# Kernel optimization log

Hardware: AMD Instinct MI355X
Metric: run time of the kernel (lower is better)

Reference implementation:

```python
import jax, jax.numpy as jnp
import numpy as np

NUM_EMBEDDINGS = 1024
EMBEDDING_DIM = 128
COMMITMENT_COST = 0.25


def setup_inputs() -> dict:
    key = jax.random.key(0)
    k_in, k_cb = jax.random.split(key)
    inputs = jax.random.normal(k_in, (8, EMBEDDING_DIM, 16, 32, 32), dtype=jnp.float32)
    # torch init: uniform_(-1/num_embeddings, 1/num_embeddings)
    codebook = jax.random.uniform(
        k_cb, (NUM_EMBEDDINGS, EMBEDDING_DIM), dtype=jnp.float32,
        minval=-1.0 / NUM_EMBEDDINGS, maxval=1.0 / NUM_EMBEDDINGS)
    return {"inputs": inputs, "codebook": codebook}


def reference(inputs, codebook):
    # inputs: [B, C, D, H, W] with C == embedding_dim; codebook: [K, C]
    C = codebook.shape[1]
    flat = jnp.transpose(inputs, (0, 2, 3, 4, 1)).reshape(-1, C)  # [N, C]
    # squared L2 distances via the expanded form (matches torch code)
    distances = (jnp.sum(flat ** 2, axis=1, keepdims=True)
                 + jnp.sum(codebook ** 2, axis=1)
                 - 2.0 * flat @ codebook.T)  # [N, K]
    encoding_indices = jnp.argmin(distances, axis=1)  # [N]
    quantized = codebook[encoding_indices]  # [N, C]
    # NOTE: faithful to original bug — plain reshape back to channels-first
    # inputs.shape with no inverse permute (torch: quantized.view(inputs.shape))
    quantized = quantized.reshape(inputs.shape)
    e_latent_loss = jnp.mean((jax.lax.stop_gradient(quantized) - inputs) ** 2)
    q_latent_loss = jnp.mean((quantized - jax.lax.stop_gradient(inputs)) ** 2)
    loss = q_latent_loss + COMMITMENT_COST * e_latent_loss
    # straight-through estimator
    quantized_st = inputs + jax.lax.stop_gradient(quantized - inputs)
    return quantized_st, loss, encoding_indices
```

## Files before the change

kernel.cpp:

```cpp
#include <hip/hip_runtime.h>

typedef unsigned short u16;
typedef __attribute__((ext_vector_type(8))) short bf16x8;
typedef __attribute__((ext_vector_type(4))) float f32x4;

#define K_CB  1024
#define N_ROWS 131072
#define NUMEL (N_ROWS * 128)
#define TAU2 6.0e-4f
#define SMALLCAP 32768
#define FULLCAP  32768

#define GLOAD16(gp, lp) __builtin_amdgcn_global_load_lds( \
    (const __attribute__((address_space(1))) unsigned int*)(gp), \
    (__attribute__((address_space(3))) unsigned int*)(lp), 16, 0, 0)

__device__ __forceinline__ u16 f2bf(float x) {
    union { float f; unsigned int u; } a; a.f = x;
    unsigned int r = a.u + 0x7fffu + ((a.u >> 16) & 1u);
    return (u16)(r >> 16);
}

__global__ void prep_cb_kernel(const float* __restrict__ cb, float* __restrict__ bn,
                               u16* __restrict__ Bpl, int* __restrict__ cnts) {
    int k = blockIdx.x * 256 + threadIdx.x;
    if (blockIdx.x == 0 && threadIdx.x < 2) cnts[threadIdx.x] = 0;
    if (k >= K_CB) return;
    const float4* row4 = reinterpret_cast<const float4*>(cb) + k * 32;
    float s = 0.f;
    #pragma unroll
    for (int i = 0; i < 32; ++i) {
        float4 v = row4[i];
        s = fmaf(v.x, v.x, s); s = fmaf(v.y, v.y, s);
        s = fmaf(v.z, v.z, s); s = fmaf(v.w, v.w, s);
    }
    bn[k] = s;
    const float* rf = cb + k * 128;
    #pragma unroll
    for (int s8 = 0; s8 < 16; ++s8) {
        unsigned int hw[8];
        #pragma unroll
        for (int j = 0; j < 8; ++j) hw[j] = f2bf(rf[s8 * 8 + j]);
        uint4 H;
        H.x = hw[0] | (hw[1] << 16); H.y = hw[2] | (hw[3] << 16);
        H.z = hw[4] | (hw[5] << 16); H.w = hw[6] | (hw[7] << 16);
        *reinterpret_cast<uint4*>(&Bpl[((size_t)s8 * 1024 + k) * 8]) = H;
    }
}

__launch_bounds__(256, 3)
__global__ void gemm_fused_kernel(const float* __restrict__ in, const float* __restrict__ cb,
                                  const u16* __restrict__ Bpl, const float* __restrict__ bn,
                                  float* __restrict__ out_q, float* __restrict__ idx_out,
                                  uint2* __restrict__ smallL, int* __restrict__ fullL,
                                  int* __restrict__ cnts,
                                  float* __restrict__ deltas, float* __restrict__ partials) {
    __shared__ u16 A_s[16 * 64 * 8];
    __shared__ u16 Bb[2 * 4 * 256 * 8];
    __shared__ float bn_s[K_CB];
    __shared__ float red_s[4];

    const int tid = threadIdx.x;
    const int w = tid >> 6, lane = tid & 63, g4 = lane >> 4, l15 = lane & 15;
    const int blk = blockIdx.x, n0 = blk * 64;

    #pragma unroll
    for (int i = 0; i < 4; ++i) {
        const u16* g = Bpl + (size_t)(w * 1024 + i * 64 + lane) * 8;
        GLOAD16(g, &Bb[(w * 256 + i * 64) * 8]);
    }
    for (int i = tid; i < K_CB; i += 256) bn_s[i] = bn[i];

    {
        const int base = (n0 >> 14) * (128 * 16384) + (n0 & 16383);
        #pragma unroll
        for (int i = 0; i < 4; ++i) {
            int p = tid + i * 256;
            int n = p & 63, s = p >> 6;
            const float* g = in + base + (size_t)(s * 8) * 16384 + n;
            unsigned int pw[8];
            #pragma unroll
            for (int j = 0; j < 8; ++j) pw[j] = f2bf(g[(size_t)j * 16384]);
            uint4 H;
            H.x = pw[0] | (pw[1] << 16); H.y = pw[2] | (pw[3] << 16);
            H.z = pw[4] | (pw[5] << 16); H.w = pw[6] | (pw[7] << 16);
            *reinterpret_cast<uint4*>(&A_s[(s * 64 + n) * 8]) = H;
        }
    }
    __syncthreads();

    f32x4 acc[4][4];
    const f32x4 zz = {0.f, 0.f, 0.f, 0.f};
    #pragma unroll
    for (int mi = 0; mi < 4; ++mi)
        #pragma unroll
        for (int ni = 0; ni < 4; ++ni) acc[mi][ni] = zz;

    float b1[16], b2[16]; int i1[16];
    #pragma unroll
    for (int sl = 0; sl < 16; ++sl) { b1[sl] = 3.4e38f; b2[sl] = 3.4e38f; i1[sl] = 0; }

    #pragma unroll
    for (int t = 0; t < 16; ++t) {
        const int chunk = t >> 2, cc = t & 3, buf = t & 1;
        if (t < 15) {
            const int t2 = t + 1, chunk2 = t2 >> 2, cc2 = t2 & 3, nb = t2 & 1;
            #pragma unroll
            for (int i = 0; i < 4; ++i) {
                const u16* g = Bpl + (size_t)((cc2 * 4 + w) * 1024 + chunk2 * 256 + i * 64 + lane) * 8;
                GLOAD16(g, &Bb[((nb * 4 + w) * 256 + i * 64) * 8]);
            }
        }
        bf16x8 af[4], bfr[4];
        #pragma unroll
        for (int mi = 0; mi < 4; ++mi)
            af[mi] = *reinterpret_cast<const bf16x8*>(
                &A_s[((cc * 4 + g4) * 64 + mi * 16 + l15) * 8]);
        #pragma unroll
        for (int ni = 0; ni < 4; ++ni)
            bfr[ni] = *reinterpret_cast<const bf16x8*>(
                &Bb[((buf * 4 + g4) * 256 + w * 64 + ni * 16 + l15) * 8]);
        #pragma unroll
        for (int mi = 0; mi < 4; ++mi)
            #pragma unroll
            for (int ni = 0; ni < 4; ++ni)
                acc[mi][ni] = __builtin_amdgcn_mfma_f32_16x16x32_bf16(af[mi], bfr[ni], acc[mi][ni], 0, 0, 0);

        if (cc == 3) {
            const int cb0s = chunk * 256;
            #pragma unroll
            for (int mi = 0; mi < 4; ++mi) {
                #pragma unroll
                for (int ni = 0; ni < 4; ++ni) {
                    int n = cb0s + w * 64 + ni * 16 + l15;
                    float bnv = bn_s[n];
                    #pragma unroll
                    for (int r = 0; r < 4; ++r) {
                        float s = fmaf(-2.0f, acc[mi][ni][r], bnv);
                        int sl = mi * 4 + r;
                        if (s < b1[sl]) { b2[sl] = b1[sl]; b1[sl] = s; i1[sl] = n; }
                        else if (s < b2[sl]) b2[sl] = s;
                    }
                    acc[mi][ni] = zz;
                }
            }
        }
        __syncthreads();
    }

    float* m_b1   = (float*)Bb;
    float* m_b2   = m_b1 + 256;
    int*   m_i1   = (int*)(m_b2 + 256);
    int*   idx_s  = m_i1 + 256;
    float* gmin_s = (float*)(idx_s + 64);
    int*   flg_s  = (int*)(gmin_s + 64);
    int*   ccnt_s = flg_s + 64;
    int*   fb_s   = ccnt_s + 64;
    int*   cand_s = fb_s + 64;

    #pragma unroll
    for (int sl = 0; sl < 16; ++sl) {
        float v1 = b1[sl], v2 = b2[sl]; int ix = i1[sl];
        #pragma unroll
        for (int m = 1; m < 16; m <<= 1) {
            float o1 = __shfl_xor(v1, m, 64);
            int   oi = __shfl_xor(ix, m, 64);
            float o2 = __shfl_xor(v2, m, 64);
            if (o1 < v1 || (o1 == v1 && oi < ix)) { v2 = fminf(v1, o2); v1 = o1; ix = oi; }
            else v2 = fminf(v2, o1);
        }
        if (l15 == 0) {
            int mi = sl >> 2, r = sl & 3;
            int rl = mi * 16 + g4 * 4 + r;
            m_b1[w * 64 + rl] = v1; m_b2[w * 64 + rl] = v2; m_i1[w * 64 + rl] = ix;
        }
    }
    __syncthreads();
    if (tid < 64) {
        float v1 = m_b1[tid], v2 = m_b2[tid]; int ix = m_i1[tid];
        #pragma unroll
        for (int wv = 1; wv < 4; ++wv) {
            float o1 = m_b1[wv * 64 + tid], o2 = m_b2[wv * 64 + tid]; int oi = m_i1[wv * 64 + tid];
            if (o1 < v1 || (o1 == v1 && oi < ix)) { v2 = fminf(v1, o2); v1 = o1; ix = oi; }
            else v2 = fminf(v2, o1);
        }
        idx_s[tid] = ix;
        idx_out[n0 + tid] = (float)ix;
        deltas[n0 + tid] = 0.f;
        gmin_s[tid] = v1;
        flg_s[tid] = (v2 - v1 <= TAU2) ? 1 : 0;
        ccnt_s[tid] = 0;
        fb_s[tid] = 0;
    }
    __syncthreads();

    #pragma unroll
    for (int sl = 0; sl < 16; ++sl) {
        int mi = sl >> 2, r = sl & 3;
        int rl = mi * 16 + g4 * 4 + r;
        if (flg_s[rl]) {
            float g = gmin_s[rl];
            if (b1[sl] - g <= TAU2) {
                int p = atomicAdd(&ccnt_s[rl], 1);
                if (p < 4) cand_s[rl * 4 + p] = i1[sl]; else fb_s[rl] = 1;
            }
            if (b2[sl] - g <= TAU2) fb_s[rl] = 1;
        }
    }
    __syncthreads();
    if (tid < 64 && flg_s[tid]) {
        int nc = ccnt_s[tid];
        int row = n0 + tid;
        if (!fb_s[tid] && nc >= 2) {
            int p = atomicAdd(&cnts[0], 1);
            if (p < SMALLCAP) {
                unsigned long long key = (unsigned long long)row |
                                         ((unsigned long long)nc << 20);
                for (int j = 0; j < nc; ++j)
                    key |= (unsigned long long)(cand_s[tid * 4 + j] & 1023) << (24 + 10 * j);
                uint2 rec; rec.x = (unsigned)key; rec.y = (unsigned)(key >> 32);
                smallL[p] = rec;
            } else {
                int q = atomicAdd(&cnts[1], 1);
                if (q < FULLCAP) fullL[q] = row;
            }
        } else if (fb_s[tid]) {
            int q = atomicAdd(&cnts[1], 1);
            if (q < FULLCAP) fullL[q] = row;
        }
    }
    __syncthreads();

    float acc_l = 0.f;
    const float4* cb4 = reinterpret_cast<const float4*>(cb);
    const float4* in4 = reinterpret_cast<const float4*>(in);
    float4* out4 = reinterpret_cast<float4*>(out_q);
    #pragma unroll
    for (int i = 0; i < 8; ++i) {
        int idx = tid + i * 256;
        int row = idx >> 5;
        int c4 = idx & 31;
        int kq = idx_s[row];
        float4 q = cb4[kq * 32 + c4];
        float4 x = in4[(size_t)(n0 + row) * 32 + c4];
        float4 d, o;
        d.x = q.x - x.x; d.y = q.y - x.y; d.z = q.z - x.z; d.w = q.w - x.w;
        o.x = x.x + d.x; o.y = x.y + d.y; o.z = x.z + d.z; o.w = x.w + d.w;
        out4[(size_t)(n0 + row) * 32 + c4] = o;
        acc_l += d.x * d.x; acc_l += d.y * d.y; acc_l += d.z * d.z; acc_l += d.w * d.w;
    }
    #pragma unroll
    for (int m = 1; m < 64; m <<= 1) acc_l += __shfl_xor(acc_l, m, 64);
    if ((tid & 63) == 0) red_s[tid >> 6] = acc_l;
    __syncthreads();
    if (tid == 0) partials[blk] = red_s[0] + red_s[1] + red_s[2] + red_s[3];
}

__device__ __forceinline__ void patch_row(const float* __restrict__ in,
                                          const float* __restrict__ cb,
                                          float* __restrict__ idx_out,
                                          float* __restrict__ out_q,
                                          float* __restrict__ deltas,
                                          int row, int k_new, int lane) {
    int k_old = (int)idx_out[row];
    if (k_new == k_old) return;
    if (lane == 0) idx_out[row] = (float)k_new;
    float dd = 0.f;
    if (lane < 32) {
        const float4* in4 = reinterpret_cast<const float4*>(in);
        const float4* cb4 = reinterpret_cast<const float4*>(cb);
        float4* out4 = reinterpret_cast<float4*>(out_q);
        float4 x = in4[(size_t)row * 32 + lane];
        float4 qn = cb4[(size_t)k_new * 32 + lane];
        float4 qo = cb4[(size_t)k_old * 32 + lane];
        float4 dn, dl, o;
        dn.x = qn.x - x.x; dn.y = qn.y - x.y; dn.z = qn.z - x.z; dn.w = qn.w - x.w;
        o.x = x.x + dn.x; o.y = x.y + dn.y; o.z = x.z + dn.z; o.w = x.w + dn.w;
        out4[(size_t)row * 32 + lane] = o;
        dl.x = qo.x - x.x; dl.y = qo.y - x.y; dl.z = qo.z - x.z; dl.w = qo.w - x.w;
        dd = dn.x * dn.x + dn.y * dn.y + dn.z * dn.z + dn.w * dn.w
           - (dl.x * dl.x + dl.y * dl.y + dl.z * dl.z + dl.w * dl.w);
    }
    #pragma unroll
    for (int m = 1; m < 64; m <<= 1) dd += __shfl_xor(dd, m, 64);
    if (lane == 0) deltas[row] = dd;
}

__global__ void small_rescore_kernel(const float* __restrict__ in, const float* __restrict__ cb,
                                     const float* __restrict__ bn, const uint2* __restrict__ recs,
                                     const int* __restrict__ cnts, float* __restrict__ idx_out,
                                     float* __restrict__ out_q, float* __restrict__ deltas) {
    __shared__ float xls[4][128];
    const int tid = threadIdx.x, wv = tid >> 6, lane = tid & 63;
    int ns = cnts[0]; if (ns > SMALLCAP) ns = SMALLCAP;
    float* xl = xls[wv];
    for (int f = blockIdx.x * 4 + wv; f < ns; f += gridDim.x * 4) {
        uint2 rc = recs[f];
        unsigned long long key = ((unsigned long long)rc.y << 32) | (unsigned long long)rc.x;
        int row = (int)(key & 131071ull);
        int nc = (int)((key >> 20) & 7ull);
        int ck = (lane < 4) ? (int)((key >> (24 + 10 * lane)) & 1023ull) : 0;
        const float* bp = in + (size_t)(row >> 14) * 2097152 + (row & 16383);
        xl[2 * lane]     = bp[(size_t)(2 * lane) * 16384];
        xl[2 * lane + 1] = bp[(size_t)(2 * lane + 1) * 16384];
        asm volatile("s_waitcnt vmcnt(0) lgkmcnt(0)" ::: "memory");
        float xn = 0.f;
        for (int c = 0; c < 128; ++c) { float v = xl[c]; xn = fmaf(v, v, xn); }
        float s = 3.4e38f; int kk = 0x7fffffff;
        if (lane < nc) {
            const float4* cr = reinterpret_cast<const float4*>(cb + (size_t)ck * 128);
            float dot = 0.f;
            #pragma unroll
            for (int c4 = 0; c4 < 32; ++c4) {
                float4 bv = cr[c4];
                float4 xv = *reinterpret_cast<const float4*>(&xl[c4 * 4]);
                dot = fmaf(xv.x, bv.x, dot); dot = fmaf(xv.y, bv.y, dot);
                dot = fmaf(xv.z, bv.z, dot); dot = fmaf(xv.w, bv.w, dot);
            }
            float t1 = xn + bn[ck];
            s = fmaf(-2.0f, dot, t1);
            kk = ck;
        }
        #pragma unroll
        for (int m = 1; m < 4; m <<= 1) {
            float os = __shfl_xor(s, m, 64);
            int ok = __shfl_xor(kk, m, 64);
            if (os < s || (os == s && ok < kk)) { s = os; kk = ok; }
        }
        int k_new = __shfl(kk, 0, 64);
        patch_row(in, cb, idx_out, out_q, deltas, row, k_new, lane);
    }
}

__global__ void full_rescore_kernel(const float* __restrict__ in, const float* __restrict__ cb,
                                    const float* __restrict__ bn, const int* __restrict__ fullL,
                                    const int* __restrict__ cnts, float* __restrict__ idx_out,
                                    float* __restrict__ out_q, float* __restrict__ deltas) {
    __shared__ float xls[4][128];
    const int tid = threadIdx.x, wv = tid >> 6, lane = tid & 63;
    int nf = cnts[1]; if (nf > FULLCAP) nf = FULLCAP;
    float* xl = xls[wv];
    for (int f = blockIdx.x * 4 + wv; f < nf; f += gridDim.x * 4) {
        int row = fullL[f];
        const float* bp = in + (size_t)(row >> 14) * 2097152 + (row & 16383);
        xl[2 * lane]     = bp[(size_t)(2 * lane) * 16384];
        xl[2 * lane + 1] = bp[(size_t)(2 * lane + 1) * 16384];
        asm volatile("s_waitcnt vmcnt(0) lgkmcnt(0)" ::: "memory");
        float xn = 0.f;
        for (int c = 0; c < 128; ++c) { float v = xl[c]; xn = fmaf(v, v, xn); }
        float best = 3.4e38f; int bi = 0x7fffffff;
        for (int j = 0; j < 16; ++j) {
            int k = j * 64 + lane;
            const float4* cr = reinterpret_cast<const float4*>(cb + (size_t)k * 128);
            float dot = 0.f;
            #pragma unroll
            for (int c4 = 0; c4 < 32; ++c4) {
                float4 bv = cr[c4];
                float4 xv = *reinterpret_cast<const float4*>(&xl[c4 * 4]);
                dot = fmaf(xv.x, bv.x, dot); dot = fmaf(xv.y, bv.y, dot);
                dot = fmaf(xv.z, bv.z, dot); dot = fmaf(xv.w, bv.w, dot);
            }
            float t1 = xn + bn[k];
            float s = fmaf(-2.0f, dot, t1);
            if (s < best || (s == best && k < bi)) { best = s; bi = k; }
        }
        #pragma unroll
        for (int m = 1; m < 64; m <<= 1) {
            float os = __shfl_xor(best, m, 64);
            int ok = __shfl_xor(bi, m, 64);
            if (os < best || (os == best && ok < bi)) { best = os; bi = ok; }
        }
        int k_new = __shfl(bi, 0, 64);
        patch_row(in, cb, idx_out, out_q, deltas, row, k_new, lane);
    }
}

__global__ void loss_stage1(const float* __restrict__ partials, const float* __restrict__ deltas,
                            float* __restrict__ part2) {
    __shared__ float red_s[4];
    const int blk = blockIdx.x, tid = threadIdx.x;
    float s = 0.f;
    const float* dp = deltas + blk * 2048;
    for (int i = tid; i < 2048; i += 256) s += dp[i];
    if (tid < 32) s += partials[blk * 32 + tid];
    #pragma unroll
    for (int m = 1; m < 64; m <<= 1) s += __shfl_xor(s, m, 64);
    if ((tid & 63) == 0) red_s[tid >> 6] = s;
    __syncthreads();
    if (tid == 0) part2[blk] = red_s[0] + red_s[1] + red_s[2] + red_s[3];
}

__global__ void loss_stage2(const float* __restrict__ part2, float* __restrict__ out_loss) {
    const int tid = threadIdx.x;
    float s = part2[tid];
    #pragma unroll
    for (int m = 1; m < 64; m <<= 1) s += __shfl_xor(s, m, 64);
    if (tid == 0) out_loss[0] = 1.25f * (s / (float)NUMEL);
}

extern "C" void kernel_launch(void* const* d_in, const int* in_sizes, int n_in,
                              void* d_out, int out_size, void* d_ws, size_t ws_size,
                              hipStream_t stream) {
    (void)in_sizes; (void)n_in; (void)out_size; (void)ws_size;
    const float* in = (const float*)d_in[0];
    const float* cb = (const float*)d_in[1];
    float* out = (float*)d_out;

    char* ws = (char*)d_ws;
    float* bn       = (float*)(ws + 0);
    u16*   Bpl      = (u16*)(ws + 4096);
    uint2* smallL   = (uint2*)(ws + 528384);
    int*   fullL    = (int*)(ws + 790528);
    float* deltas   = (float*)(ws + 921600);
    float* partials = (float*)(ws + 1445888);
    float* part2    = (float*)(ws + 1454080);
    int*   cnts     = (int*)(ws + 1454336);

    float* idxf = out + NUMEL + 1;

    prep_cb_kernel<<<4, 256, 0, stream>>>(cb, bn, Bpl, cnts);
    gemm_fused_kernel<<<2048, 256, 0, stream>>>(in, cb, Bpl, bn, out, idxf,
                                                smallL, fullL, cnts, deltas, partials);
    small_rescore_kernel<<<1024, 256, 0, stream>>>(in, cb, bn, smallL, cnts, idxf, out, deltas);
    full_rescore_kernel<<<256, 256, 0, stream>>>(in, cb, bn, fullL, cnts, idxf, out, deltas);
    loss_stage1<<<64, 256, 0, stream>>>(partials, deltas, part2);
    loss_stage2<<<1, 64, 0, stream>>>(part2, out + NUMEL);
}
```

Before: 308.4 us.

## Split-wait barriers in MFMA loop and aggregate list atomics per block

```diff
diff --git a/kernel.cpp b/kernel.cpp
--- a/kernel.cpp
+++ b/kernel.cpp
@@ -110,7 +110,12 @@
                 const u16* g = Bpl + (size_t)((cc2 * 4 + w) * 1024 + chunk2 * 256 + i * 64 + lane) * 8;
                 GLOAD16(g, &Bb[((nb * 4 + w) * 256 + i * 64) * 8]);
             }
-        }
+            asm volatile("s_waitcnt vmcnt(4)" ::: "memory");
+        } else {
+            asm volatile("s_waitcnt vmcnt(0)" ::: "memory");
+        }
+        __builtin_amdgcn_s_barrier();
+
         bf16x8 af[4], bfr[4];
         #pragma unroll
         for (int mi = 0; mi < 4; ++mi)
@@ -124,16 +129,16 @@
         for (int mi = 0; mi < 4; ++mi)
             #pragma unroll
             for (int ni = 0; ni < 4; ++ni)
-                acc[mi][ni] = __builtin_amdgcn_mfma_f32_16x16x32_bf16(af[mi], bfr[ni], acc[mi][ni], 0, 0, 0);
+                acc[mi][ni] = __builtin_amdgcn_mfma_f32_16x16x32_bf16(
+                    af[mi], bfr[ni], acc[mi][ni], 0, 0, 0);
 
         if (cc == 3) {
-            const int cb0s = chunk * 256;
-            #pragma unroll
-            for (int mi = 0; mi < 4; ++mi) {
+            #pragma unroll
+            for (int ni = 0; ni < 4; ++ni) {
+                int n = chunk * 256 + w * 64 + ni * 16 + l15;
+                float bnv = bn_s[n];
                 #pragma unroll
-                for (int ni = 0; ni < 4; ++ni) {
-                    int n = cb0s + w * 64 + ni * 16 + l15;
-                    float bnv = bn_s[n];
+                for (int mi = 0; mi < 4; ++mi) {
                     #pragma unroll
                     for (int r = 0; r < 4; ++r) {
                         float s = fmaf(-2.0f, acc[mi][ni][r], bnv);
@@ -145,7 +150,8 @@
                 }
             }
         }
-        __syncthreads();
+        asm volatile("s_waitcnt lgkmcnt(0)" ::: "memory");
+        __builtin_amdgcn_s_barrier();
     }
 
     float* m_b1   = (float*)Bb;
@@ -157,6 +163,9 @@
     int*   ccnt_s = flg_s + 64;
     int*   fb_s   = ccnt_s + 64;
     int*   cand_s = fb_s + 64;
+    uint2* sRec_s = (uint2*)(cand_s + 256);
+    int*   fRow_s = (int*)(sRec_s + 64);
+    int*   aux_s  = fRow_s + 64;
 
     #pragma unroll
     for (int sl = 0; sl < 16; ++sl) {
@@ -191,6 +200,7 @@
         flg_s[tid] = (v2 - v1 <= TAU2) ? 1 : 0;
         ccnt_s[tid] = 0;
         fb_s[tid] = 0;
+        if (tid < 2) aux_s[tid] = 0;
     }
     __syncthreads();
 
@@ -208,26 +218,38 @@
         }
     }
     __syncthreads();
+
     if (tid < 64 && flg_s[tid]) {
         int nc = ccnt_s[tid];
         int row = n0 + tid;
         if (!fb_s[tid] && nc >= 2) {
-            int p = atomicAdd(&cnts[0], 1);
-            if (p < SMALLCAP) {
-                unsigned long long key = (unsigned long long)row |
-                                         ((unsigned long long)nc << 20);
-                for (int j = 0; j < nc; ++j)
-                    key |= (unsigned long long)(cand_s[tid * 4 + j] & 1023) << (24 + 10 * j);
-                uint2 rec; rec.x = (unsigned)key; rec.y = (unsigned)(key >> 32);
-                smallL[p] = rec;
-            } else {
-                int q = atomicAdd(&cnts[1], 1);
-                if (q < FULLCAP) fullL[q] = row;
-            }
+            unsigned long long key = (unsigned long long)row |
+                                     ((unsigned long long)nc << 20);
+            for (int j = 0; j < nc; ++j)
+                key |= (unsigned long long)(cand_s[tid * 4 + j] & 1023) << (24 + 10 * j);
+            int p = atomicAdd(&aux_s[0], 1);
+            uint2 rec; rec.x = (unsigned)key; rec.y = (unsigned)(key >> 32);
+            sRec_s[p] = rec;
         } else if (fb_s[tid]) {
+            int q = atomicAdd(&aux_s[1], 1);
+            fRow_s[q] = row;
+        }
+    }
+    __syncthreads();
+    if (tid == 0)  aux_s[2] = (aux_s[0] > 0) ? atomicAdd(&cnts[0], aux_s[0]) : 0;
+    if (tid == 64) aux_s[3] = (aux_s[1] > 0) ? atomicAdd(&cnts[1], aux_s[1]) : 0;
+    __syncthreads();
+    if (tid < aux_s[0]) {
+        int p = aux_s[2] + tid;
+        if (p < SMALLCAP) smallL[p] = sRec_s[tid];
+        else {
             int q = atomicAdd(&cnts[1], 1);
-            if (q < FULLCAP) fullL[q] = row;
-        }
+            if (q < FULLCAP) fullL[q] = (int)(sRec_s[tid].x & 131071u);
+        }
+    }
+    if (tid >= 64 && tid < 128 && (tid - 64) < aux_s[1]) {
+        int p = aux_s[3] + (tid - 64);
+        if (p < FULLCAP) fullL[p] = fRow_s[tid - 64];
     }
     __syncthreads();
 
@@ -251,7 +273,7 @@
     }
     #pragma unroll
     for (int m = 1; m < 64; m <<= 1) acc_l += __shfl_xor(acc_l, m, 64);
-    if ((tid & 63) == 0) red_s[tid >> 6] = acc_l;
+    if (lane == 0) red_s[w] = acc_l;
     __syncthreads();
     if (tid == 0) partials[blk] = red_s[0] + red_s[1] + red_s[2] + red_s[3];
 }
```

New measurement: 289.3 us. 1.07x faster.
